# Optimization experiments

Hardware: AMD Instinct MI355X
Metric: run time of the kernel (lower is better)

The kernel has to match this reference:

```python
import jax, jax.numpy as jnp
import numpy as np

E, K, D, H, C = 32768, 32, 128, 4, 10
DH = D // H

def setup_inputs() -> dict:
    key = jax.random.key(0)
    ks = jax.random.split(key, 9)
    s = 1.0 / np.sqrt(D)
    return {
        "edge_feats": jax.random.normal(ks[0], (E, D), jnp.float32),
        "Wq": jax.random.normal(ks[1], (D, D), jnp.float32) * s,
        "Wk": jax.random.normal(ks[2], (D, D), jnp.float32) * s,
        "Wv": jax.random.normal(ks[3], (D, D), jnp.float32) * s,
        "Wo": jax.random.normal(ks[4], (D, D), jnp.float32) * s,
        "W1": jax.random.normal(ks[5], (D, D), jnp.float32) * s,
        "b1": jnp.zeros((D,), jnp.float32),
        "W2": jax.random.normal(ks[6], (D, C), jnp.float32) * s,
        "b2": jnp.zeros((C,), jnp.float32),
        "edge_adj": jax.random.randint(ks[7], (E, K), 0, E, jnp.int32),
    }

def reference(edge_feats, Wq, Wk, Wv, Wo, W1, b1, W2, b2, edge_adj):
    # Edge attention: each edge attends over its K adjacent edges.
    q = (edge_feats @ Wq).reshape(E, H, DH)                 # [E,H,dh]
    k_all = edge_feats @ Wk                                  # [E,D]
    v_all = edge_feats @ Wv                                  # [E,D]
    kn = k_all[edge_adj].reshape(E, K, H, DH)                # gather [E,K,H,dh]
    vn = v_all[edge_adj].reshape(E, K, H, DH)                # gather [E,K,H,dh]
    scores = jnp.einsum("ehd,ekhd->ehk", q, kn) / np.sqrt(DH)
    attn = jax.nn.softmax(scores, axis=-1)                   # [E,H,K]
    ctx = jnp.einsum("ehk,ekhd->ehd", attn, vn).reshape(E, D)
    edge_out = ctx @ Wo                                       # [E,D]
    # classifier: Linear -> GELU -> Linear
    h = jax.nn.gelu(edge_out @ W1 + b1)
    logits = h @ W2 + b2                                      # [E,C]
    return logits
```

## Files before the change

### kernel.cpp

```cpp
#include <hip/hip_runtime.h>
#include <hip/hip_bf16.h>

constexpr int E_EDGES = 32768;
constexpr int DIM = 128;

using bf16x8 = __attribute__((ext_vector_type(8))) short;
using f32x4  = __attribute__((ext_vector_type(4))) float;
using f32x2  = __attribute__((ext_vector_type(2))) float;
typedef unsigned int uint4v __attribute__((ext_vector_type(4)));
typedef unsigned int uint2v __attribute__((ext_vector_type(2)));

__device__ inline float bflo(unsigned u) { return __uint_as_float(u << 16); }
__device__ inline float bfhi(unsigned u) { return __uint_as_float(u & 0xffff0000u); }
__device__ inline f32x2 bf2f2(unsigned u) {
    f32x2 r;
    r[0] = __uint_as_float(u << 16);
    r[1] = __uint_as_float(u & 0xffff0000u);
    return r;
}
__device__ inline f32x2 fma2(f32x2 a, f32x2 b, f32x2 c) {
    return __builtin_elementwise_fma(a, b, c);
}
__device__ inline unsigned pk_bf2(float a, float b) {
    __hip_bfloat162 h = __float22bfloat162_rn(make_float2(a, b));
    return *(unsigned*)&h;
}

#if __has_builtin(__builtin_amdgcn_fdot2_f32_bf16)
typedef __bf16 bf16x2v __attribute__((ext_vector_type(2)));
__device__ inline float dot2bf(unsigned a, unsigned b, float c) {
    return __builtin_amdgcn_fdot2_f32_bf16(__builtin_bit_cast(bf16x2v, a),
                                           __builtin_bit_cast(bf16x2v, b),
                                           c, false);
}
#else
__device__ inline float dot2bf(unsigned a, unsigned b, float c) {
    float r = fmaf(bflo(a), bflo(b), c);
    return fmaf(bfhi(a), bfhi(b), r);
}
#endif

__global__ __launch_bounds__(256) void k_prep(
    const float* __restrict__ Wq, const float* __restrict__ Wk,
    const float* __restrict__ Wv, const float* __restrict__ Wo,
    const float* __restrict__ W1, __hip_bfloat16* __restrict__ Wt,
    __hip_bfloat16* __restrict__ wft) {
    const int b = blockIdx.x;
    const int t = threadIdx.x;
    if (b < 3) {
        const float* W = (b == 0) ? Wq : (b == 1) ? Wk : Wv;
        __hip_bfloat16* dst = Wt + b * 16384;
#pragma unroll
        for (int i = 0; i < 8; ++i) {
            int idx = i * 2048 + t * 8;
            int k = idx >> 7, n0 = idx & 127;
            float4 f0 = *(const float4*)(W + k * 128 + n0);
            float4 f1 = *(const float4*)(W + k * 128 + n0 + 4);
            float f[8] = {f0.x, f0.y, f0.z, f0.w, f1.x, f1.y, f1.z, f1.w};
#pragma unroll
            for (int j = 0; j < 8; ++j)
                dst[(n0 + j) * 128 + k] = __float2bfloat16(f[j]);
        }
    } else {
        int idx = (b - 3) * 256 + t;
        int r = idx >> 7, c = idx & 127;
        float acc = 0.f;
#pragma unroll 16
        for (int k = 0; k < 128; ++k)
            acc = fmaf(Wo[r * 128 + k], W1[k * 128 + c], acc);
        wft[c * 128 + r] = __float2bfloat16(acc);
    }
}

__global__ __launch_bounds__(256) void k_qkv(
    const float* __restrict__ feats, const __hip_bfloat16* __restrict__ Wt,
    __hip_bfloat16* __restrict__ qp, __hip_bfloat16* __restrict__ kp,
    __hip_bfloat16* __restrict__ vp) {
    __shared__ short Als[16384];
    __shared__ short Bls[16384];

    const int t = threadIdx.x;
    const int lane = t & 63;
    const int w = t >> 6;
    const int wm = w >> 1, wn = w & 1;
    const int row0 = blockIdx.x * 128;

#pragma unroll
    for (int i = 0; i < 8; ++i) {
        int idx = i * 2048 + t * 8;
        int r = idx >> 7, k0 = idx & 127;
        float4 f0 = *(const float4*)(feats + (size_t)(row0 + r) * DIM + k0);
        float4 f1 = *(const float4*)(feats + (size_t)(row0 + r) * DIM + k0 + 4);
        uint4 o = make_uint4(pk_bf2(f0.x, f0.y), pk_bf2(f0.z, f0.w),
                             pk_bf2(f1.x, f1.y), pk_bf2(f1.z, f1.w));
        *(uint4*)&Als[(r * 128 + k0) ^ ((r & 7) << 3)] = o;
    }
#pragma unroll
    for (int i = 0; i < 8; ++i) {
        int idx = i * 2048 + t * 8;
        int n = idx >> 7, k0 = idx & 127;
        uint4 v = *(const uint4*)(Wt + n * 128 + k0);
        *(uint4*)&Bls[(n * 128 + k0) ^ ((n & 7) << 3)] = v;
    }
    __syncthreads();

    bf16x8 afr[4][4];
#pragma unroll
    for (int m = 0; m < 4; ++m)
#pragma unroll
        for (int ks = 0; ks < 4; ++ks) {
            int r = wm * 64 + m * 16 + (lane & 15);
            int kb = ks * 32 + (lane >> 4) * 8;
            afr[m][ks] = *(bf16x8*)&Als[(r * 128 + kb) ^ ((r & 7) << 3)];
        }

    for (int proj = 0; proj < 3; ++proj) {
        f32x4 acc[4][4];
#pragma unroll
        for (int m = 0; m < 4; ++m)
#pragma unroll
            for (int n = 0; n < 4; ++n) acc[m][n] = (f32x4){0.f, 0.f, 0.f, 0.f};

#pragma unroll
        for (int ks = 0; ks < 4; ++ks) {
            bf16x8 bfr[4];
#pragma unroll
            for (int n = 0; n < 4; ++n) {
                int nn = wn * 64 + n * 16 + (lane & 15);
                int kb = ks * 32 + (lane >> 4) * 8;
                bfr[n] = *(bf16x8*)&Bls[(nn * 128 + kb) ^ ((nn & 7) << 3)];
            }
#pragma unroll
            for (int m = 0; m < 4; ++m)
#pragma unroll
                for (int n = 0; n < 4; ++n)
                    acc[m][n] = __builtin_amdgcn_mfma_f32_16x16x32_bf16(
                        afr[m][ks], bfr[n], acc[m][n], 0, 0, 0);
        }

        {
            __hip_bfloat16* dst = (proj == 0) ? qp : (proj == 1) ? kp : vp;
#pragma unroll
            for (int n = 0; n < 4; ++n) {
                int c = wn * 64 + n * 16 + (lane & 15);
                int h = c >> 5, pr = h & 1;
                int slot = ((h >> 1) << 5) + (c & 31);
                size_t base = (size_t)pr * E_EDGES * 64 + slot;
#pragma unroll
                for (int m = 0; m < 4; ++m) {
                    int rb = row0 + wm * 64 + m * 16 + (lane >> 4) * 4;
#pragma unroll
                    for (int r = 0; r < 4; ++r)
                        dst[base + (size_t)(rb + r) * 64] =
                            __float2bfloat16(acc[m][n][r]);
                }
            }
        }

        if (proj < 2) {
            __syncthreads();
#pragma unroll
            for (int i = 0; i < 8; ++i) {
                int idx = i * 2048 + t * 8;
                int n = idx >> 7, k0 = idx & 127;
                uint4 v = *(const uint4*)(Wt + (proj + 1) * 16384 + n * 128 + k0);
                *(uint4*)&Bls[(n * 128 + k0) ^ ((n & 7) << 3)] = v;
            }
            __syncthreads();
        }
    }
}

__global__ __launch_bounds__(256) void k_attn(
    const __hip_bfloat16* __restrict__ qp, const __hip_bfloat16* __restrict__ kp,
    const __hip_bfloat16* __restrict__ vp, const int* __restrict__ adj,
    __hip_bfloat16* __restrict__ ctxb) {
    const int pass = blockIdx.y;
    const int lane = threadIdx.x & 63;
    const int e = blockIdx.x * 4 + (threadIdx.x >> 6);
    const int n = lane & 31;
    const int g = lane >> 5;

    int adjv = 0;
    if (lane < 32) adjv = __builtin_nontemporal_load(adj + e * 32 + lane);

    const uint4v* qr =
        (const uint4v*)(qp + ((size_t)pass * E_EDGES + e) * 64 + g * 32);
    uint4v qu[4];
#pragma unroll
    for (int j = 0; j < 4; ++j) qu[j] = __builtin_nontemporal_load(qr + j);

    const int row = __shfl(adjv, n, 64);
    const uint4* kr =
        (const uint4*)(kp + ((size_t)pass * E_EDGES + row) * 64 + g * 32);
    float s0 = 0.f;
#pragma unroll
    for (int j = 0; j < 4; ++j) {
        uint4 u = kr[j];
        s0 = dot2bf(qu[j][0], u.x, s0);
        s0 = dot2bf(qu[j][1], u.y, s0);
        s0 = dot2bf(qu[j][2], u.z, s0);
        s0 = dot2bf(qu[j][3], u.w, s0);
    }
    s0 *= 0.17677669529663689f;

    float m0 = s0;
#pragma unroll
    for (int off = 16; off; off >>= 1) m0 = fmaxf(m0, __shfl_xor(m0, off));
    float e0 = __expf(s0 - m0);
    float sum0 = e0;
#pragma unroll
    for (int off = 16; off; off >>= 1) sum0 += __shfl_xor(sum0, off);
    const float wgt = e0 / sum0;

    const int rsel = lane >> 3;
    const int csel = lane & 7;
    const int gi = csel >> 2;
    f32x2 c01 = {0.f, 0.f}, c23 = {0.f, 0.f}, c45 = {0.f, 0.f}, c67 = {0.f, 0.f};
#pragma unroll
    for (int i = 0; i < 4; ++i) {
        int nn = i * 8 + rsel;
        float a = __shfl(wgt, gi * 32 + nn, 64);
        int r2 = __shfl(adjv, nn, 64);
        uint4 u = *(const uint4*)(vp + ((size_t)pass * E_EDGES + r2) * 64 + csel * 8);
        f32x2 a2 = {a, a};
        c01 = fma2(a2, bf2f2(u.x), c01);
        c23 = fma2(a2, bf2f2(u.y), c23);
        c45 = fma2(a2, bf2f2(u.z), c45);
        c67 = fma2(a2, bf2f2(u.w), c67);
    }
    float c[8] = {c01[0], c01[1], c23[0], c23[1], c45[0], c45[1], c67[0], c67[1]};
#pragma unroll
    for (int off = 8; off <= 32; off <<= 1)
#pragma unroll
        for (int j = 0; j < 8; ++j) c[j] += __shfl_xor(c[j], off);

    if (lane < 8) {
        int h2 = pass + 2 * (lane >> 2);
        uint4v o;
        o[0] = pk_bf2(c[0], c[1]);
        o[1] = pk_bf2(c[2], c[3]);
        o[2] = pk_bf2(c[4], c[5]);
        o[3] = pk_bf2(c[6], c[7]);
        __builtin_nontemporal_store(
            o, (uint4v*)(ctxb + (size_t)e * DIM + h2 * 32 + (lane & 3) * 8));
    }
}

__global__ __launch_bounds__(256) void k_mlp(
    const __hip_bfloat16* __restrict__ ctxb, const __hip_bfloat16* __restrict__ wft,
    const float* __restrict__ b1, const float* __restrict__ W2,
    const float* __restrict__ b2, float* __restrict__ out) {
    __shared__ short Als[16384];
    __shared__ short Bls[16384];
    __shared__ float w2s[1280];
    __shared__ float b1s[128];
    __shared__ float b2s[16];

    const int t = threadIdx.x;
    const int lane = t & 63;
    const int w = t >> 6;
    const int wm = w >> 1, wn = w & 1;
    const int row0 = blockIdx.x * 128;

#pragma unroll
    for (int i = 0; i < 8; ++i) {
        int idx = i * 2048 + t * 8;
        int r = idx >> 7, k0 = idx & 127;
        uint4 v = *(const uint4*)(ctxb + (size_t)(row0 + r) * DIM + k0);
        *(uint4*)&Als[(r * 128 + k0) ^ ((r & 7) << 3)] = v;
    }
#pragma unroll
    for (int i = 0; i < 8; ++i) {
        int idx = i * 2048 + t * 8;
        int n = idx >> 7, k0 = idx & 127;
        uint4 v = *(const uint4*)(wft + n * 128 + k0);
        *(uint4*)&Bls[(n * 128 + k0) ^ ((n & 7) << 3)] = v;
    }
    for (int i = t; i < 1280; i += 256) w2s[i] = W2[i];
    if (t < 128) b1s[t] = b1[t];
    if (t < 10) b2s[t] = b2[t];
    __syncthreads();

    f32x4 acc[4][4];
#pragma unroll
    for (int m = 0; m < 4; ++m)
#pragma unroll
        for (int n = 0; n < 4; ++n) acc[m][n] = (f32x4){0.f, 0.f, 0.f, 0.f};

#pragma unroll
    for (int ks = 0; ks < 4; ++ks) {
        bf16x8 afr[4], bfr[4];
#pragma unroll
        for (int m = 0; m < 4; ++m) {
            int r = wm * 64 + m * 16 + (lane & 15);
            int kb = ks * 32 + (lane >> 4) * 8;
            afr[m] = *(bf16x8*)&Als[(r * 128 + kb) ^ ((r & 7) << 3)];
        }
#pragma unroll
        for (int n = 0; n < 4; ++n) {
            int nn = wn * 64 + n * 16 + (lane & 15);
            int kb = ks * 32 + (lane >> 4) * 8;
            bfr[n] = *(bf16x8*)&Bls[(nn * 128 + kb) ^ ((nn & 7) << 3)];
        }
#pragma unroll
        for (int m = 0; m < 4; ++m)
#pragma unroll
            for (int n = 0; n < 4; ++n)
                acc[m][n] = __builtin_amdgcn_mfma_f32_16x16x32_bf16(
                    afr[m], bfr[n], acc[m][n], 0, 0, 0);
    }

    __syncthreads();
#pragma unroll
    for (int m = 0; m < 4; ++m) {
        int lr0 = wm * 64 + m * 16 + (lane >> 4) * 4;
#pragma unroll
        for (int n = 0; n < 4; ++n) {
            int c = wn * 64 + n * 16 + (lane & 15);
            float bc = b1s[c];
#pragma unroll
            for (int r = 0; r < 4; ++r) {
                float x = acc[m][n][r] + bc;
                float u = 0.7978845608028654f * (x + 0.044715f * x * x * x);
                float ex = __expf(2.f * u);
                float th = 1.f - 2.f / (ex + 1.f);
                float h = 0.5f * x * (1.f + th);
                int lr = lr0 + r;
                Als[(lr * 128 + c) ^ ((lr & 7) << 3)] =
                    (short)(__bfloat16_as_ushort(__float2bfloat16(h)));
            }
        }
    }
    __syncthreads();

    {
        int r = t >> 1;
        int c0 = (t & 1) * 5;
        float a0 = b2s[c0], a1 = b2s[c0 + 1], a2 = b2s[c0 + 2],
              a3 = b2s[c0 + 3], a4 = b2s[c0 + 4];
#pragma unroll 8
        for (int kk = 0; kk < 128; ++kk) {
            float hv = __uint_as_float(
                ((unsigned)(unsigned short)Als[(r * 128 + kk) ^ ((r & 7) << 3)]) << 16);
            const float* wrow = &w2s[kk * 10 + c0];
            a0 = fmaf(hv, wrow[0], a0);
            a1 = fmaf(hv, wrow[1], a1);
            a2 = fmaf(hv, wrow[2], a2);
            a3 = fmaf(hv, wrow[3], a3);
            a4 = fmaf(hv, wrow[4], a4);
        }
        float* o = out + (size_t)(row0 + r) * 10 + c0;
        o[0] = a0; o[1] = a1; o[2] = a2; o[3] = a3; o[4] = a4;
    }
}

extern "C" void kernel_launch(void* const* d_in, const int* in_sizes, int n_in,
                              void* d_out, int out_size, void* d_ws, size_t ws_size,
                              hipStream_t stream) {
    const float* feats = (const float*)d_in[0];
    const float* Wq    = (const float*)d_in[1];
    const float* Wk    = (const float*)d_in[2];
    const float* Wv    = (const float*)d_in[3];
    const float* Wo    = (const float*)d_in[4];
    const float* W1    = (const float*)d_in[5];
    const float* b1    = (const float*)d_in[6];
    const float* W2    = (const float*)d_in[7];
    const float* b2    = (const float*)d_in[8];
    const int*   adj   = (const int*)d_in[9];
    float* out = (float*)d_out;

    const size_t ED2 = (size_t)E_EDGES * 64;
    __hip_bfloat16* base = (__hip_bfloat16*)d_ws;
    __hip_bfloat16* qp   = base;
    __hip_bfloat16* kp   = qp + 2 * ED2;
    __hip_bfloat16* vp   = kp + 2 * ED2;
    __hip_bfloat16* ctxb = vp + 2 * ED2;
    __hip_bfloat16* wt   = ctxb + 2 * ED2;
    __hip_bfloat16* wft  = wt + 3 * 16384;

    k_prep<<<67, 256, 0, stream>>>(Wq, Wk, Wv, Wo, W1, wt, wft);
    k_qkv<<<E_EDGES / 128, 256, 0, stream>>>(feats, wt, qp, kp, vp);
    k_attn<<<dim3(E_EDGES / 4, 2), 256, 0, stream>>>(qp, kp, vp, adj, ctxb);
    k_mlp<<<E_EDGES / 128, 256, 0, stream>>>(ctxb, wft, b1, W2, b2, out);
}
```

Before: 96.89 us.

## Fuse attention and classifier MLP into one kernel via shared-memory context tiles

Merges the attention kernel and the MLP kernel into one. Each 256-thread block handles 16 edges: its waves compute the per-head context into shared memory, then run the fused Wo·W1 GEMM with MFMA (B fragments read straight from global), apply GELU and do the final 10-class projection. This removes the bf16 context round trip through global memory and one kernel launch. In exchange each block loops serially over 8 edge-head units per wave, reloads W2, the biases and the weight fragments for every 16 edges, and the last stage uses only 160 threads.

```diff
diff --git a/kernel.cpp b/kernel.cpp
--- a/kernel.cpp
+++ b/kernel.cpp
@@ -171,187 +171,156 @@
     }
 }
 
-__global__ __launch_bounds__(256) void k_attn(
+__global__ __launch_bounds__(256) void k_attn_mlp(
     const __hip_bfloat16* __restrict__ qp, const __hip_bfloat16* __restrict__ kp,
     const __hip_bfloat16* __restrict__ vp, const int* __restrict__ adj,
-    __hip_bfloat16* __restrict__ ctxb) {
-    const int pass = blockIdx.y;
-    const int lane = threadIdx.x & 63;
-    const int e = blockIdx.x * 4 + (threadIdx.x >> 6);
+    const __hip_bfloat16* __restrict__ wft, const float* __restrict__ b1,
+    const float* __restrict__ W2, const float* __restrict__ b2,
+    float* __restrict__ out) {
+    __shared__ short ctxls[2048];
+    __shared__ short hls[2048];
+    __shared__ float w2s[1280];
+    __shared__ float b1s[128];
+    __shared__ float b2s[16];
+
+    const int t = threadIdx.x;
+    const int lane = t & 63;
+    const int w = t >> 6;
+    const int e0 = blockIdx.x * 16;
+
+    for (int i = t; i < 1280; i += 256) w2s[i] = W2[i];
+    if (t < 128) b1s[t] = b1[t];
+    if (t < 10) b2s[t] = b2[t];
+
     const int n = lane & 31;
     const int g = lane >> 5;
-
-    int adjv = 0;
-    if (lane < 32) adjv = __builtin_nontemporal_load(adj + e * 32 + lane);
-
-    const uint4v* qr =
-        (const uint4v*)(qp + ((size_t)pass * E_EDGES + e) * 64 + g * 32);
-    uint4v qu[4];
-#pragma unroll
-    for (int j = 0; j < 4; ++j) qu[j] = __builtin_nontemporal_load(qr + j);
-
-    const int row = __shfl(adjv, n, 64);
-    const uint4* kr =
-        (const uint4*)(kp + ((size_t)pass * E_EDGES + row) * 64 + g * 32);
-    float s0 = 0.f;
-#pragma unroll
-    for (int j = 0; j < 4; ++j) {
-        uint4 u = kr[j];
-        s0 = dot2bf(qu[j][0], u.x, s0);
-        s0 = dot2bf(qu[j][1], u.y, s0);
-        s0 = dot2bf(qu[j][2], u.z, s0);
-        s0 = dot2bf(qu[j][3], u.w, s0);
-    }
-    s0 *= 0.17677669529663689f;
-
-    float m0 = s0;
-#pragma unroll
-    for (int off = 16; off; off >>= 1) m0 = fmaxf(m0, __shfl_xor(m0, off));
-    float e0 = __expf(s0 - m0);
-    float sum0 = e0;
-#pragma unroll
-    for (int off = 16; off; off >>= 1) sum0 += __shfl_xor(sum0, off);
-    const float wgt = e0 / sum0;
-
     const int rsel = lane >> 3;
     const int csel = lane & 7;
     const int gi = csel >> 2;
-    f32x2 c01 = {0.f, 0.f}, c23 = {0.f, 0.f}, c45 = {0.f, 0.f}, c67 = {0.f, 0.f};
-#pragma unroll
-    for (int i = 0; i < 4; ++i) {
-        int nn = i * 8 + rsel;
-        float a = __shfl(wgt, gi * 32 + nn, 64);
-        int r2 = __shfl(adjv, nn, 64);
-        uint4 u = *(const uint4*)(vp + ((size_t)pass * E_EDGES + r2) * 64 + csel * 8);
-        f32x2 a2 = {a, a};
-        c01 = fma2(a2, bf2f2(u.x), c01);
-        c23 = fma2(a2, bf2f2(u.y), c23);
-        c45 = fma2(a2, bf2f2(u.z), c45);
-        c67 = fma2(a2, bf2f2(u.w), c67);
-    }
-    float c[8] = {c01[0], c01[1], c23[0], c23[1], c45[0], c45[1], c67[0], c67[1]};
-#pragma unroll
-    for (int off = 8; off <= 32; off <<= 1)
-#pragma unroll
-        for (int j = 0; j < 8; ++j) c[j] += __shfl_xor(c[j], off);
-
-    if (lane < 8) {
-        int h2 = pass + 2 * (lane >> 2);
-        uint4v o;
-        o[0] = pk_bf2(c[0], c[1]);
-        o[1] = pk_bf2(c[2], c[3]);
-        o[2] = pk_bf2(c[4], c[5]);
-        o[3] = pk_bf2(c[6], c[7]);
-        __builtin_nontemporal_store(
-            o, (uint4v*)(ctxb + (size_t)e * DIM + h2 * 32 + (lane & 3) * 8));
-    }
-}
-
-__global__ __launch_bounds__(256) void k_mlp(
-    const __hip_bfloat16* __restrict__ ctxb, const __hip_bfloat16* __restrict__ wft,
-    const float* __restrict__ b1, const float* __restrict__ W2,
-    const float* __restrict__ b2, float* __restrict__ out) {
-    __shared__ short Als[16384];
-    __shared__ short Bls[16384];
-    __shared__ float w2s[1280];
-    __shared__ float b1s[128];
-    __shared__ float b2s[16];
-
-    const int t = threadIdx.x;
-    const int lane = t & 63;
-    const int w = t >> 6;
-    const int wm = w >> 1, wn = w & 1;
-    const int row0 = blockIdx.x * 128;
-
-#pragma unroll
-    for (int i = 0; i < 8; ++i) {
-        int idx = i * 2048 + t * 8;
-        int r = idx >> 7, k0 = idx & 127;
-        uint4 v = *(const uint4*)(ctxb + (size_t)(row0 + r) * DIM + k0);
-        *(uint4*)&Als[(r * 128 + k0) ^ ((r & 7) << 3)] = v;
-    }
-#pragma unroll
-    for (int i = 0; i < 8; ++i) {
-        int idx = i * 2048 + t * 8;
-        int n = idx >> 7, k0 = idx & 127;
-        uint4 v = *(const uint4*)(wft + n * 128 + k0);
-        *(uint4*)&Bls[(n * 128 + k0) ^ ((n & 7) << 3)] = v;
-    }
-    for (int i = t; i < 1280; i += 256) w2s[i] = W2[i];
-    if (t < 128) b1s[t] = b1[t];
-    if (t < 10) b2s[t] = b2[t];
+
+    for (int it = 0; it < 8; ++it) {
+        const int u = w * 8 + it;
+        const int pass = u >> 4;
+        const int eloc = u & 15;
+        const int e = e0 + eloc;
+
+        int adjv = 0;
+        if (lane < 32) adjv = __builtin_nontemporal_load(adj + e * 32 + lane);
+
+        const uint4v* qr =
+            (const uint4v*)(qp + ((size_t)pass * E_EDGES + e) * 64 + g * 32);
+        uint4v qu[4];
+#pragma unroll
+        for (int j = 0; j < 4; ++j) qu[j] = __builtin_nontemporal_load(qr + j);
+
+        const int row = __shfl(adjv, n, 64);
+        const uint4* kr =
+            (const uint4*)(kp + ((size_t)pass * E_EDGES + row) * 64 + g * 32);
+        float s0 = 0.f;
+#pragma unroll
+        for (int j = 0; j < 4; ++j) {
+            uint4 uu = kr[j];
+            s0 = dot2bf(qu[j][0], uu.x, s0);
+            s0 = dot2bf(qu[j][1], uu.y, s0);
+            s0 = dot2bf(qu[j][2], uu.z, s0);
+            s0 = dot2bf(qu[j][3], uu.w, s0);
+        }
+        s0 *= 0.17677669529663689f;
+
+        float m0 = s0;
+#pragma unroll
+        for (int off = 16; off; off >>= 1) m0 = fmaxf(m0, __shfl_xor(m0, off));
+        float ex0 = __expf(s0 - m0);
+        float sum0 = ex0;
+#pragma unroll
+        for (int off = 16; off; off >>= 1) sum0 += __shfl_xor(sum0, off);
+        const float wgt = ex0 / sum0;
+
+        f32x2 c01 = {0.f, 0.f}, c23 = {0.f, 0.f}, c45 = {0.f, 0.f}, c67 = {0.f, 0.f};
+#pragma unroll
+        for (int i = 0; i < 4; ++i) {
+            int nn = i * 8 + rsel;
+            float a = __shfl(wgt, gi * 32 + nn, 64);
+            int r2 = __shfl(adjv, nn, 64);
+            uint4 uu = *(const uint4*)(vp + ((size_t)pass * E_EDGES + r2) * 64 + csel * 8);
+            f32x2 a2 = {a, a};
+            c01 = fma2(a2, bf2f2(uu.x), c01);
+            c23 = fma2(a2, bf2f2(uu.y), c23);
+            c45 = fma2(a2, bf2f2(uu.z), c45);
+            c67 = fma2(a2, bf2f2(uu.w), c67);
+        }
+        float c[8] = {c01[0], c01[1], c23[0], c23[1], c45[0], c45[1], c67[0], c67[1]};
+#pragma unroll
+        for (int off = 8; off <= 32; off <<= 1)
+#pragma unroll
+            for (int j = 0; j < 8; ++j) c[j] += __shfl_xor(c[j], off);
+
+        if (lane < 8) {
+            int h2 = pass + 2 * (lane >> 2);
+            uint4v o;
+            o[0] = pk_bf2(c[0], c[1]);
+            o[1] = pk_bf2(c[2], c[3]);
+            o[2] = pk_bf2(c[4], c[5]);
+            o[3] = pk_bf2(c[6], c[7]);
+            *(uint4v*)&ctxls[(eloc * 128 + h2 * 32 + (lane & 3) * 8) ^
+                             ((eloc & 7) << 3)] = o;
+        }
+    }
     __syncthreads();
 
-    f32x4 acc[4][4];
-#pragma unroll
-    for (int m = 0; m < 4; ++m)
-#pragma unroll
-        for (int n = 0; n < 4; ++n) acc[m][n] = (f32x4){0.f, 0.f, 0.f, 0.f};
-
-#pragma unroll
-    for (int ks = 0; ks < 4; ++ks) {
-        bf16x8 afr[4], bfr[4];
-#pragma unroll
-        for (int m = 0; m < 4; ++m) {
-            int r = wm * 64 + m * 16 + (lane & 15);
+    {
+        const int lr = lane & 15;
+        bf16x8 afr[4], bfr[2][4];
+#pragma unroll
+        for (int ks = 0; ks < 4; ++ks) {
             int kb = ks * 32 + (lane >> 4) * 8;
-            afr[m] = *(bf16x8*)&Als[(r * 128 + kb) ^ ((r & 7) << 3)];
-        }
-#pragma unroll
-        for (int n = 0; n < 4; ++n) {
-            int nn = wn * 64 + n * 16 + (lane & 15);
-            int kb = ks * 32 + (lane >> 4) * 8;
-            bfr[n] = *(bf16x8*)&Bls[(nn * 128 + kb) ^ ((nn & 7) << 3)];
-        }
-#pragma unroll
-        for (int m = 0; m < 4; ++m)
-#pragma unroll
-            for (int n = 0; n < 4; ++n)
-                acc[m][n] = __builtin_amdgcn_mfma_f32_16x16x32_bf16(
-                    afr[m], bfr[n], acc[m][n], 0, 0, 0);
-    }
-
+            afr[ks] = *(bf16x8*)&ctxls[(lr * 128 + kb) ^ ((lr & 7) << 3)];
+        }
+#pragma unroll
+        for (int nf = 0; nf < 2; ++nf)
+#pragma unroll
+            for (int ks = 0; ks < 4; ++ks) {
+                int nn2 = w * 32 + nf * 16 + (lane & 15);
+                int kb = ks * 32 + (lane >> 4) * 8;
+                bfr[nf][ks] = *(const bf16x8*)(wft + nn2 * 128 + kb);
+            }
+        f32x4 acc[2] = {(f32x4){0.f, 0.f, 0.f, 0.f}, (f32x4){0.f, 0.f, 0.f, 0.f}};
+#pragma unroll
+        for (int ks = 0; ks < 4; ++ks) {
+            acc[0] = __builtin_amdgcn_mfma_f32_16x16x32_bf16(afr[ks], bfr[0][ks],
+                                                             acc[0], 0, 0, 0);
+            acc[1] = __builtin_amdgcn_mfma_f32_16x16x32_bf16(afr[ks], bfr[1][ks],
+                                                             acc[1], 0, 0, 0);
+        }
+#pragma unroll
+        for (int nf = 0; nf < 2; ++nf) {
+            int c = w * 32 + nf * 16 + (lane & 15);
+            float bc = b1s[c];
+#pragma unroll
+            for (int r = 0; r < 4; ++r) {
+                float x = acc[nf][r] + bc;
+                float uu = 0.7978845608028654f * (x + 0.044715f * x * x * x);
+                float exu = __expf(2.f * uu);
+                float th = 1.f - 2.f / (exu + 1.f);
+                float h = 0.5f * x * (1.f + th);
+                int hr = (lane >> 4) * 4 + r;
+                hls[(hr * 128 + c) ^ ((hr & 7) << 3)] =
+                    (short)(__bfloat16_as_ushort(__float2bfloat16(h)));
+            }
+        }
+    }
     __syncthreads();
-#pragma unroll
-    for (int m = 0; m < 4; ++m) {
-        int lr0 = wm * 64 + m * 16 + (lane >> 4) * 4;
-#pragma unroll
-        for (int n = 0; n < 4; ++n) {
-            int c = wn * 64 + n * 16 + (lane & 15);
-            float bc = b1s[c];
-#pragma unroll
-            for (int r = 0; r < 4; ++r) {
-                float x = acc[m][n][r] + bc;
-                float u = 0.7978845608028654f * (x + 0.044715f * x * x * x);
-                float ex = __expf(2.f * u);
-                float th = 1.f - 2.f / (ex + 1.f);
-                float h = 0.5f * x * (1.f + th);
-                int lr = lr0 + r;
-                Als[(lr * 128 + c) ^ ((lr & 7) << 3)] =
-                    (short)(__bfloat16_as_ushort(__float2bfloat16(h)));
-            }
-        }
-    }
-    __syncthreads();
-
-    {
-        int r = t >> 1;
-        int c0 = (t & 1) * 5;
-        float a0 = b2s[c0], a1 = b2s[c0 + 1], a2 = b2s[c0 + 2],
-              a3 = b2s[c0 + 3], a4 = b2s[c0 + 4];
+
+    if (t < 160) {
+        int r = t / 10, c = t - r * 10;
+        float a = b2s[c];
 #pragma unroll 8
         for (int kk = 0; kk < 128; ++kk) {
             float hv = __uint_as_float(
-                ((unsigned)(unsigned short)Als[(r * 128 + kk) ^ ((r & 7) << 3)]) << 16);
-            const float* wrow = &w2s[kk * 10 + c0];
-            a0 = fmaf(hv, wrow[0], a0);
-            a1 = fmaf(hv, wrow[1], a1);
-            a2 = fmaf(hv, wrow[2], a2);
-            a3 = fmaf(hv, wrow[3], a3);
-            a4 = fmaf(hv, wrow[4], a4);
-        }
-        float* o = out + (size_t)(row0 + r) * 10 + c0;
-        o[0] = a0; o[1] = a1; o[2] = a2; o[3] = a3; o[4] = a4;
+                ((unsigned)(unsigned short)hls[(r * 128 + kk) ^ ((r & 7) << 3)]) << 16);
+            a = fmaf(hv, w2s[kk * 10 + c], a);
+        }
+        out[(size_t)(e0 + r) * 10 + c] = a;
     }
 }
 
@@ -375,12 +344,11 @@
     __hip_bfloat16* qp   = base;
     __hip_bfloat16* kp   = qp + 2 * ED2;
     __hip_bfloat16* vp   = kp + 2 * ED2;
-    __hip_bfloat16* ctxb = vp + 2 * ED2;
-    __hip_bfloat16* wt   = ctxb + 2 * ED2;
+    __hip_bfloat16* wt   = vp + 2 * ED2;
     __hip_bfloat16* wft  = wt + 3 * 16384;
 
     k_prep<<<67, 256, 0, stream>>>(Wq, Wk, Wv, Wo, W1, wt, wft);
     k_qkv<<<E_EDGES / 128, 256, 0, stream>>>(feats, wt, qp, kp, vp);
-    k_attn<<<dim3(E_EDGES / 4, 2), 256, 0, stream>>>(qp, kp, vp, adj, ctxb);
-    k_mlp<<<E_EDGES / 128, 256, 0, stream>>>(ctxb, wft, b1, W2, b2, out);
-}
+    k_attn_mlp<<<E_EDGES / 16, 256, 0, stream>>>(qp, kp, vp, adj, wft,
+                                                 b1, W2, b2, out);
+}
```

After: 116.9 us. 20.7% more time.
